# Kernel optimization log

Measured on AMD Instinct MI355X. Metric: run time of the kernel, lower is better.

Reference implementation:

```python
import jax, jax.numpy as jnp
import numpy as np

B, S, D, C = 2, 4096, 768, 8192
SCALE = 1.0
LN_EPS = 1e-5


def setup_inputs() -> dict:
    key = jax.random.key(0)
    ks = jax.random.split(key, 8)
    std = 0.03
    return {
        "x": jax.random.normal(ks[0], (B, S, D), dtype=jnp.float32),
        "attention_masks": jax.random.randint(ks[1], (B, S), 0, 2).astype(jnp.int32),
        "Wk": jax.random.normal(ks[2], (D, D), dtype=jnp.float32) * std,
        "Wv": jax.random.normal(ks[3], (D, D), dtype=jnp.float32) * std,
        "bv": jnp.zeros((D,), dtype=jnp.float32),
        "Q": jax.random.normal(ks[4], (C, D), dtype=jnp.float32) * std,  # label_representations
        "ln_gamma": jnp.ones((D,), dtype=jnp.float32),
        "ln_beta": jnp.zeros((D,), dtype=jnp.float32),
        "w_out": jax.random.normal(ks[5], (D,), dtype=jnp.float32) * std,  # output_linear.weight [1, D]
        "b_out": jnp.zeros((), dtype=jnp.float32),  # output_linear.bias [1]
    }


def reference(x, attention_masks, Wk, Wv, bv, Q, ln_gamma, ln_beta, w_out, b_out):
    # K, V projections (torch Linear: x @ W.T + b)
    K = jnp.einsum("bsd,ed->bse", x, Wk)
    V = jnp.einsum("bsd,ed->bse", x, Wv) + bv
    # label-query cross-attention scores: [B, C, S]
    scores = jnp.einsum("cd,bsd->bcs", Q, K)
    # additive mask: -inf where attention_masks == 0 (intended semantics of pad/repeat/masked_fill)
    scores = jnp.where(attention_masks[:, None, :] == 0, -jnp.inf, scores)
    attn = jax.nn.softmax(scores / SCALE, axis=2)  # [B, C, S]
    y = jnp.einsum("bcs,bsd->bcd", attn, V)  # [B, C, D]
    # LayerNorm over last dim
    mu = jnp.mean(y, axis=-1, keepdims=True)
    var = jnp.mean((y - mu) ** 2, axis=-1, keepdims=True)
    y = (y - mu) * jax.lax.rsqrt(var + LN_EPS) * ln_gamma + ln_beta
    # elementwise weight-mul-sum output head: [B, C]
    return jnp.einsum("bcd,d->bc", y, w_out) + b_out
```

## Files before the change

kernel.cpp:

```cpp
#include <hip/hip_runtime.h>
#include <hip/hip_bf16.h>
#include <hip/hip_fp16.h>

typedef _Float16 f16x8 __attribute__((ext_vector_type(8)));
typedef _Float16 f16x4 __attribute__((ext_vector_type(4)));
typedef float f32x4 __attribute__((ext_vector_type(4)));

#define AS1 __attribute__((address_space(1)))
#define AS3 __attribute__((address_space(3)))
#define MFMA16(a, b, c) __builtin_amdgcn_mfma_f32_16x16x32_f16(a, b, c, 0, 0, 0)

#define LDP 2304

__global__ __launch_bounds__(256) void maskscan(const int* __restrict__ am,
                                                int* __restrict__ idx,
                                                int* __restrict__ meta) {
  const int b = blockIdx.x, t = threadIdx.x;
  const int* m = am + (size_t)b * 4096;
  int* ix = idx + (size_t)b * 4096;
  __shared__ int cnt[256];
  __shared__ int pre[257];
  int loc[16], c = 0;
#pragma unroll
  for (int j = 0; j < 16; ++j) {
    loc[j] = m[t * 16 + j];
    c += (loc[j] != 0);
  }
  cnt[t] = c;
  __syncthreads();
  if (t == 0) {
    pre[0] = 0;
    for (int i = 0; i < 256; ++i) pre[i + 1] = pre[i] + cnt[i];
  }
  __syncthreads();
  int p = pre[t];
#pragma unroll
  for (int j = 0; j < 16; ++j)
    if (loc[j]) ix[p++] = t * 16 + j;
  const int valid = pre[256];
  int nsp = ((valid + 255) >> 8) << 8;
  if (nsp < 512) nsp = 512;
  for (int j = valid + t; j < nsp; j += 256) ix[j] = -1;
  if (t == 0) { meta[2 * b] = valid; meta[2 * b + 1] = nsp; }
}

__global__ __launch_bounds__(192) void gather_cvt(const float* __restrict__ x,
                                                  const int* __restrict__ idx,
                                                  const int* __restrict__ meta,
                                                  unsigned short* __restrict__ xc) {
  const int b = blockIdx.y, row = blockIdx.x, t = threadIdx.x;
  if (row >= meta[2 * b + 1]) return;
  const int src = idx[(size_t)b * 4096 + row];
  unsigned short* dst = xc + ((size_t)b * 4096 + row) * 768 + t * 4;
  f16x4 h;
  if (src < 0) {
    h[0] = h[1] = h[2] = h[3] = (_Float16)0.0f;
  } else {
    float4 v = *(const float4*)(x + ((size_t)b * 4096 + src) * 768 + t * 4);
    h[0] = (_Float16)v.x; h[1] = (_Float16)v.y; h[2] = (_Float16)v.z; h[3] = (_Float16)v.w;
  }
  *(f16x4*)dst = h;
}

__global__ __launch_bounds__(256) void cvt_f32_f16(const float* __restrict__ in,
                                                   unsigned short* __restrict__ out,
                                                   int n8) {
  int i = blockIdx.x * 256 + threadIdx.x;
  if (i >= n8) return;
  const float4* p = (const float4*)in + 2 * (size_t)i;
  float4 a = p[0], b = p[1];
  f16x8 h;
  h[0] = (_Float16)a.x; h[1] = (_Float16)a.y; h[2] = (_Float16)a.z; h[3] = (_Float16)a.w;
  h[4] = (_Float16)b.x; h[5] = (_Float16)b.y; h[6] = (_Float16)b.z; h[7] = (_Float16)b.w;
  *(f16x8*)(out + (size_t)i * 8) = h;
}

template <int OMODE, bool RBIAS, int EXITD>
__global__ __launch_bounds__(256) void gemm_nt(const unsigned short* __restrict__ A, int lda,
                                               const unsigned short* __restrict__ B, int ldb,
                                               void* __restrict__ Cout, int ldc,
                                               const float* __restrict__ bias,
                                               const int* __restrict__ meta,
                                               int N, int K) {
  const int nbn = N >> 7;
  const int bm = blockIdx.x / nbn, bn = blockIdx.x % nbn;
  if constexpr (EXITD == 1) {
    if (((bm & 31) << 7) >= meta[2 * (bm >> 5) + 1]) return;
  } else if constexpr (EXITD == 2) {
    if (((bn & 31) << 7) >= meta[2 * (bn >> 5) + 1]) return;
  }
  __shared__ __attribute__((aligned(16))) unsigned short As[128 * 64];
  __shared__ __attribute__((aligned(16))) unsigned short Bs[128 * 64];
  const int tid = threadIdx.x;
  const int w = tid >> 6, l = tid & 63;
  const int wr = w >> 1, wc = w & 1;
  const int lr = l & 15, lg = l >> 4;

  const unsigned short* Ab = A + (size_t)bm * 128 * lda;
  const unsigned short* Bb = B + (size_t)bn * 128 * ldb;

  f32x4 acc[4][4] = {};

  auto ldfrag = [&](const unsigned short* base, int row, int kk) {
    int off = row * 128 + kk * 64 + lg * 16;
    off ^= (row & 7) << 4;
    return *(const f16x8*)((const unsigned char*)base + off);
  };

  for (int kt = 0; kt < K; kt += 64) {
#pragma unroll
    for (int i = 0; i < 4; ++i) {
      const int c = i * 256 + w * 64 + l;
      const int row = c >> 3, col = (((c & 7) ^ (row & 7)) << 3);
      __builtin_amdgcn_global_load_lds((const AS1 void*)(Ab + (size_t)row * lda + kt + col),
                                       (AS3 void*)(As + (i * 256 + w * 64) * 8), 16, 0, 0);
    }
#pragma unroll
    for (int i = 0; i < 4; ++i) {
      const int c = i * 256 + w * 64 + l;
      const int row = c >> 3, col = (((c & 7) ^ (row & 7)) << 3);
      __builtin_amdgcn_global_load_lds((const AS1 void*)(Bb + (size_t)row * ldb + kt + col),
                                       (AS3 void*)(Bs + (i * 256 + w * 64) * 8), 16, 0, 0);
    }
    __syncthreads();
#pragma unroll
    for (int kk = 0; kk < 2; ++kk) {
      f16x8 af[4], bf[4];
#pragma unroll
      for (int mi = 0; mi < 4; ++mi) af[mi] = ldfrag(As, wr * 64 + mi * 16 + lr, kk);
#pragma unroll
      for (int ni = 0; ni < 4; ++ni) bf[ni] = ldfrag(Bs, wc * 64 + ni * 16 + lr, kk);
#pragma unroll
      for (int mi = 0; mi < 4; ++mi)
#pragma unroll
        for (int ni = 0; ni < 4; ++ni)
          acc[mi][ni] = MFMA16(af[mi], bf[ni], acc[mi][ni]);
    }
    __syncthreads();
  }

#pragma unroll
  for (int mi = 0; mi < 4; ++mi) {
#pragma unroll
    for (int r = 0; r < 4; ++r) {
      const int row = bm * 128 + wr * 64 + mi * 16 + lg * 4 + r;
      const float badd = RBIAS ? bias[row] : 0.0f;
#pragma unroll
      for (int ni = 0; ni < 4; ++ni) {
        const int col = bn * 128 + wc * 64 + ni * 16 + lr;
        float v = acc[mi][ni][r] + badd;
        if constexpr (OMODE == 0)
          ((unsigned short*)Cout)[(size_t)row * ldc + col] =
              __builtin_bit_cast(unsigned short, (_Float16)v);
        else
          ((float*)Cout)[(size_t)row * ldc + col] = v;
      }
    }
  }
}

#define VM8 asm volatile("s_waitcnt vmcnt(8)" ::: "memory")
#define VM4 asm volatile("s_waitcnt vmcnt(4)" ::: "memory")
#define VM0 asm volatile("s_waitcnt vmcnt(0)" ::: "memory")
#define VMNONE ((void)0)
#define BARRIER asm volatile("s_barrier" ::: "memory")

#define PH(kk, mh, VMW)                                                        \
  {                                                                            \
    f16x8 a0 = ldA8(4 * (mh) + 0, (kk));                                       \
    f16x8 a1 = ldA8(4 * (mh) + 1, (kk));                                       \
    f16x8 a2 = ldA8(4 * (mh) + 2, (kk));                                       \
    f16x8 a3 = ldA8(4 * (mh) + 3, (kk));                                       \
    f16x8 b0 = ldB8(0, (kk));                                                  \
    f16x8 b1 = ldB8(1, (kk));                                                  \
    f16x8 b2 = ldB8(2, (kk));                                                  \
    f16x8 b3 = ldB8(3, (kk));                                                  \
    if (u < NT4) stage(u);                                                     \
    ++u;                                                                       \
    BARRIER;                                                                   \
    __builtin_amdgcn_s_setprio(1);                                             \
    acc[4 * (mh) + 0][0] = MFMA16(a0, b0, acc[4 * (mh) + 0][0]);               \
    acc[4 * (mh) + 0][1] = MFMA16(a0, b1, acc[4 * (mh) + 0][1]);               \
    acc[4 * (mh) + 0][2] = MFMA16(a0, b2, acc[4 * (mh) + 0][2]);               \
    acc[4 * (mh) + 0][3] = MFMA16(a0, b3, acc[4 * (mh) + 0][3]);               \
    acc[4 * (mh) + 1][0] = MFMA16(a1, b0, acc[4 * (mh) + 1][0]);               \
    acc[4 * (mh) + 1][1] = MFMA16(a1, b1, acc[4 * (mh) + 1][1]);               \
    acc[4 * (mh) + 1][2] = MFMA16(a1, b2, acc[4 * (mh) + 1][2]);               \
    acc[4 * (mh) + 1][3] = MFMA16(a1, b3, acc[4 * (mh) + 1][3]);               \
    acc[4 * (mh) + 2][0] = MFMA16(a2, b0, acc[4 * (mh) + 2][0]);               \
    acc[4 * (mh) + 2][1] = MFMA16(a2, b1, acc[4 * (mh) + 2][1]);               \
    acc[4 * (mh) + 2][2] = MFMA16(a2, b2, acc[4 * (mh) + 2][2]);               \
    acc[4 * (mh) + 2][3] = MFMA16(a2, b3, acc[4 * (mh) + 2][3]);               \
    acc[4 * (mh) + 3][0] = MFMA16(a3, b0, acc[4 * (mh) + 3][0]);               \
    acc[4 * (mh) + 3][1] = MFMA16(a3, b1, acc[4 * (mh) + 3][1]);               \
    acc[4 * (mh) + 3][2] = MFMA16(a3, b2, acc[4 * (mh) + 3][2]);               \
    acc[4 * (mh) + 3][3] = MFMA16(a3, b3, acc[4 * (mh) + 3][3]);               \
    __builtin_amdgcn_s_setprio(0);                                             \
    VMW;                                                                       \
    BARRIER;                                                                   \
  }

template <int EPI>
__global__ __launch_bounds__(512, 2) void gemm256(
    const unsigned short* __restrict__ A, int lda, size_t sAz,
    const unsigned short* __restrict__ B, int ldb, size_t sBz,
    unsigned short* __restrict__ Cout, int ldc, size_t sCz, size_t sCk,
    const int* __restrict__ meta, int NTfix) {
  __shared__ __attribute__((aligned(16))) unsigned char lds[131072];
  const int tid = threadIdx.x;
  const int wv = tid >> 6, l = tid & 63;
  const int wm = wv >> 2, wn = wv & 3;
  const int lr = l & 15, lg = l >> 4;

  const int bid = blockIdx.x;
  int z, bm, bn, NT, koff, ks = 0;
  if constexpr (EPI == 2) {
    const int L0 = (meta[1] >> 8) << 5, L1 = (meta[3] >> 8) << 5;
    int idxq;
    if (bid < L0) { z = 0; idxq = bid; }
    else if (bid < L0 + L1) { z = 1; idxq = bid - L0; }
    else return;
    bm = idxq & 31;
    bn = idxq >> 5;
    NT = NTfix;
    koff = 0;
  } else {
    z = bid / 384;
    const int r = bid - z * 384;
    ks = r / 96;
    const int q = r - ks * 96;
    bm = q & 31;
    bn = q >> 5;
    const int nsp = meta[2 * z + 1];
    NT = nsp >> 8;
    koff = ks * (nsp >> 2);
  }
  const int valid = meta[2 * z];

  const unsigned short* Ab = A + (size_t)z * sAz + koff + (size_t)bm * 256 * lda;
  const unsigned short* Bb = B + (size_t)z * sBz + koff + (size_t)bn * 256 * ldb;

  const int NT4 = NT * 4;
  int bufOff = 0;

  auto stage = [&](int uu) {
    const int tau = uu >> 2, r = uu & 3;
    const int regionOff = ((tau & 1) << 16) | ((r & 1) << 15) | ((r >> 1) << 14);
    const unsigned short* base = (r & 1) ? Bb : Ab;
    const int ld = (r & 1) ? ldb : lda;
    const int kcol0 = tau * 64 + ((r >> 1) << 5);
#pragma unroll
    for (int j = 0; j < 2; ++j) {
      const int row = wv * 32 + j * 16 + (l >> 2);
      const int col = kcol0 + ((((l & 3) ^ ((row >> 1) & 3))) << 3);
      __builtin_amdgcn_global_load_lds(
          (const AS1 void*)(base + (size_t)row * ld + col),
          (AS3 void*)(lds + regionOff + wv * 2048 + j * 1024), 16, 0, 0);
    }
  };
  auto ldA8 = [&](int mf, int kk) {
    const int row = wm * 128 + mf * 16 + lr;
    int off = (row << 6) + (lg << 4);
    off ^= ((row >> 1) & 3) << 4;
    return *(const f16x8*)(lds + bufOff + (kk << 14) + off);
  };
  auto ldB8 = [&](int nf, int kk) {
    const int row = wn * 64 + nf * 16 + lr;
    int off = (row << 6) + (lg << 4);
    off ^= ((row >> 1) & 3) << 4;
    return *(const f16x8*)(lds + bufOff + 32768 + (kk << 14) + off);
  };

  f32x4 acc[8][4] = {};

  for (int i = 0; i < 6; ++i) stage(i);
  int u = 6;
  VM8;
  BARRIER;

  for (int t = 0; t + 2 < NT; ++t) {
    bufOff = (t & 1) << 16;
    PH(0, 0, VMNONE);
    PH(0, 1, VM8);
    PH(1, 0, VMNONE);
    PH(1, 1, VM8);
  }
  bufOff = ((NT - 2) & 1) << 16;
  PH(0, 0, VMNONE);
  PH(0, 1, VM8);
  PH(1, 0, VMNONE);
  PH(1, 1, VM4);
  bufOff = ((NT - 1) & 1) << 16;
  PH(0, 0, VMNONE);
  PH(0, 1, VM0);
  PH(1, 0, VMNONE);
  PH(1, 1, VMNONE);

  const size_t crow0 = (size_t)bm * 256 + wm * 128;
  const int ccol0 = bn * 256 + wn * 64;
  unsigned short* Cz = Cout + (size_t)z * sCz + (size_t)ks * sCk;
#pragma unroll
  for (int mf = 0; mf < 8; ++mf) {
#pragma unroll
    for (int rr = 0; rr < 4; ++rr) {
      const size_t rb = (crow0 + mf * 16 + lg * 4 + rr) * (size_t)ldc;
#pragma unroll
      for (int nf = 0; nf < 4; ++nf) {
        const int col = ccol0 + nf * 16 + lr;
        float v = acc[mf][nf][rr];
        if constexpr (EPI == 2) v = (col < valid) ? __expf(v) : 0.0f;
        Cz[rb + col] = __builtin_bit_cast(unsigned short, (_Float16)v);
      }
    }
  }
}

__device__ inline float block_sum(float v, float* sh, int t) {
#pragma unroll
  for (int o = 32; o; o >>= 1) v += __shfl_xor(v, o);
  __syncthreads();
  if ((t & 63) == 0) sh[t >> 6] = v;
  __syncthreads();
  return sh[0] + sh[1] + sh[2] + sh[3];
}

__global__ __launch_bounds__(256) void ln_head(const unsigned short* __restrict__ yp,
                                               size_t zoff, size_t koff,
                                               const float* __restrict__ gam,
                                               const float* __restrict__ bet,
                                               const float* __restrict__ wo,
                                               const float* __restrict__ bo,
                                               float* __restrict__ out) {
  const int z = blockIdx.y;
  const size_t rbase = (size_t)z * zoff + (size_t)blockIdx.x * 768;
  const _Float16* y0 = (const _Float16*)yp + rbase;
  const _Float16* y1 = y0 + koff;
  const _Float16* y2 = y1 + koff;
  const _Float16* y3 = y2 + koff;
  const int t = threadIdx.x;
  float a0 = (float)y0[t] + (float)y1[t] + (float)y2[t] + (float)y3[t];
  float a1 = (float)y0[t + 256] + (float)y1[t + 256] + (float)y2[t + 256] + (float)y3[t + 256];
  float a2 = (float)y0[t + 512] + (float)y1[t + 512] + (float)y2[t + 512] + (float)y3[t + 512];
  __shared__ float sh[4];
  float s = block_sum(a0 + a1 + a2, sh, t);
  float mu = s * (1.0f / 768.0f);
  float d0 = a0 - mu, d1 = a1 - mu, d2 = a2 - mu;
  float q = block_sum(d0 * d0 + d1 * d1 + d2 * d2, sh, t);
  float rs = rsqrtf(q * (1.0f / 768.0f) + 1e-5f);
  float o = (d0 * rs * gam[t] + bet[t]) * wo[t] +
            (d1 * rs * gam[t + 256] + bet[t + 256]) * wo[t + 256] +
            (d2 * rs * gam[t + 512] + bet[t + 512]) * wo[t + 512];
  o = block_sum(o, sh, t);
  if (t == 0) out[(size_t)z * 8192 + blockIdx.x] = o + bo[0];
}

extern "C" void kernel_launch(void* const* d_in, const int* in_sizes, int n_in,
                              void* d_out, int out_size, void* d_ws, size_t ws_size,
                              hipStream_t stream) {
  const float* x  = (const float*)d_in[0];
  const int*   am = (const int*)d_in[1];
  const float* Wk = (const float*)d_in[2];
  const float* Wv = (const float*)d_in[3];
  const float* bv = (const float*)d_in[4];
  const float* Q  = (const float*)d_in[5];
  const float* gam = (const float*)d_in[6];
  const float* bet = (const float*)d_in[7];
  const float* wo  = (const float*)d_in[8];
  const float* bo  = (const float*)d_in[9];
  float* out = (float*)d_out;

  const int S = 4096, D = 768, C = 8192;
  const size_t nX = (size_t)2 * S * D;
  const size_t nW = (size_t)D * D;
  const size_t nQ = (size_t)C * D;
  const size_t nPc = (size_t)C * LDP;
  const size_t nY = (size_t)C * D;

  unsigned short* xc  = (unsigned short*)d_ws;
  unsigned short* Wkb = xc + nX;
  unsigned short* Wvb = Wkb + nW;
  unsigned short* Qb  = Wvb + nW;
  unsigned short* Kb  = Qb + nQ;
  unsigned short* Vt  = Kb + nX;
  unsigned short* P   = Vt + nX;
  unsigned short* yp  = P + 2 * nPc;
  int* idx  = (int*)(yp + 8 * nY);
  int* meta = idx + 2 * 4096;

  maskscan<<<2, 256, 0, stream>>>(am, idx, meta);
  gather_cvt<<<dim3(4096, 2), 192, 0, stream>>>(x, idx, meta, xc);

  cvt_f32_f16<<<(int)(nW / 8 / 256), 256, 0, stream>>>(Wk, Wkb, (int)(nW / 8));
  cvt_f32_f16<<<(int)(nW / 8 / 256), 256, 0, stream>>>(Wv, Wvb, (int)(nW / 8));
  cvt_f32_f16<<<(int)(nQ / 8 / 256), 256, 0, stream>>>(Q, Qb, (int)(nQ / 8));

  gemm_nt<0, false, 1><<<(8192 / 128) * (768 / 128), 256, 0, stream>>>(
      xc, D, Wkb, D, Kb, D, nullptr, meta, 768, D);
  gemm_nt<0, true, 2><<<(768 / 128) * (8192 / 128), 256, 0, stream>>>(
      Wvb, D, xc, D, Vt, 2 * S, bv, meta, 2 * S, D);

  gemm256<2><<<dim3(1024, 1), 512, 0, stream>>>(
      Qb, D, 0, Kb, D, (size_t)S * D, P, LDP, nPc, 0, meta, 12);

  gemm256<0><<<dim3(768, 1), 512, 0, stream>>>(
      P, LDP, nPc, Vt, 2 * S, (size_t)S, yp, D, 4 * nY, nY, meta, 0);

  ln_head<<<dim3(C, 2), 256, 0, stream>>>(yp, 4 * nY, nY, gam, bet, wo, bo, out);
}
```

Baseline: 243.1 us.

## Make score GEMM persistent over two tile passes and halve split-K for PV GEMM

The QK^T score GEMM now launches 512 blocks, each handling up to two output tiles in sequence: a first pass over the first 8 column tiles per batch, then the remaining valid tiles. Before, a launch of 1024 blocks had many early exits. The P·V GEMM drops split-K from 4 to 2, so it uses 384 blocks, writes half as many partial buffers, and LN reads two partials instead of four. The goal is less launch, tail and partial-sum traffic, at the cost of fewer concurrent blocks and longer per-block K loops.

Measured after the change: 234.3 us. -3.6%, faster.

```diff
diff --git a/kernel.cpp b/kernel.cpp
--- a/kernel.cpp
+++ b/kernel.cpp
@@ -213,34 +213,9 @@
   const int lr = l & 15, lg = l >> 4;
 
   const int bid = blockIdx.x;
-  int z, bm, bn, NT, koff, ks = 0;
-  if constexpr (EPI == 2) {
-    const int L0 = (meta[1] >> 8) << 5, L1 = (meta[3] >> 8) << 5;
-    int idxq;
-    if (bid < L0) { z = 0; idxq = bid; }
-    else if (bid < L0 + L1) { z = 1; idxq = bid - L0; }
-    else return;
-    bm = idxq & 31;
-    bn = idxq >> 5;
-    NT = NTfix;
-    koff = 0;
-  } else {
-    z = bid / 384;
-    const int r = bid - z * 384;
-    ks = r / 96;
-    const int q = r - ks * 96;
-    bm = q & 31;
-    bn = q >> 5;
-    const int nsp = meta[2 * z + 1];
-    NT = nsp >> 8;
-    koff = ks * (nsp >> 2);
-  }
-  const int valid = meta[2 * z];
-
-  const unsigned short* Ab = A + (size_t)z * sAz + koff + (size_t)bm * 256 * lda;
-  const unsigned short* Bb = B + (size_t)z * sBz + koff + (size_t)bn * 256 * ldb;
-
-  const int NT4 = NT * 4;
+
+  const unsigned short* Ab = nullptr;
+  const unsigned short* Bb = nullptr;
   int bufOff = 0;
 
   auto stage = [&](int uu) {
@@ -271,45 +246,86 @@
     return *(const f16x8*)(lds + bufOff + 32768 + (kk << 14) + off);
   };
 
-  f32x4 acc[8][4] = {};
-
-  for (int i = 0; i < 6; ++i) stage(i);
-  int u = 6;
-  VM8;
-  BARRIER;
-
-  for (int t = 0; t + 2 < NT; ++t) {
-    bufOff = (t & 1) << 16;
+  constexpr int NPASS = (EPI == 2) ? 2 : 1;
+
+  for (int pass = 0; pass < NPASS; ++pass) {
+    int z, bm, bn, NT, koff, ks = 0;
+    if constexpr (EPI == 2) {
+      if (pass == 0) {
+        z = bid >> 8;
+        const int rem = bid & 255;
+        bm = rem & 31;
+        bn = rem >> 5;
+        if (bn * 256 >= meta[2 * z + 1]) continue;
+      } else {
+        const int tn0 = max(0, (meta[1] >> 8) - 8);
+        const int tn1 = max(0, (meta[3] >> 8) - 8);
+        if (bid >= 32 * (tn0 + tn1)) break;
+        int t = bid;
+        if (t < 32 * tn0) { z = 0; }
+        else { t -= 32 * tn0; z = 1; }
+        bm = t & 31;
+        bn = 8 + (t >> 5);
+      }
+      NT = NTfix;
+      koff = 0;
+    } else {
+      z = bid / 192;
+      const int r = bid - z * 192;
+      ks = r / 96;
+      const int q = r - ks * 96;
+      bm = q & 31;
+      bn = q >> 5;
+      const int nsp = meta[2 * z + 1];
+      NT = nsp >> 7;
+      koff = ks * (nsp >> 1);
+    }
+    const int valid = meta[2 * z];
+
+    Ab = A + (size_t)z * sAz + koff + (size_t)bm * 256 * lda;
+    Bb = B + (size_t)z * sBz + koff + (size_t)bn * 256 * ldb;
+
+    const int NT4 = NT * 4;
+    f32x4 acc[8][4] = {};
+
+    for (int i = 0; i < 6; ++i) stage(i);
+    int u = 6;
+    VM8;
+    BARRIER;
+
+    for (int t = 0; t + 2 < NT; ++t) {
+      bufOff = (t & 1) << 16;
+      PH(0, 0, VMNONE);
+      PH(0, 1, VM8);
+      PH(1, 0, VMNONE);
+      PH(1, 1, VM8);
+    }
+    bufOff = ((NT - 2) & 1) << 16;
     PH(0, 0, VMNONE);
     PH(0, 1, VM8);
     PH(1, 0, VMNONE);
-    PH(1, 1, VM8);
-  }
-  bufOff = ((NT - 2) & 1) << 16;
-  PH(0, 0, VMNONE);
-  PH(0, 1, VM8);
-  PH(1, 0, VMNONE);
-  PH(1, 1, VM4);
-  bufOff = ((NT - 1) & 1) << 16;
-  PH(0, 0, VMNONE);
-  PH(0, 1, VM0);
-  PH(1, 0, VMNONE);
-  PH(1, 1, VMNONE);
-
-  const size_t crow0 = (size_t)bm * 256 + wm * 128;
-  const int ccol0 = bn * 256 + wn * 64;
-  unsigned short* Cz = Cout + (size_t)z * sCz + (size_t)ks * sCk;
-#pragma unroll
-  for (int mf = 0; mf < 8; ++mf) {
-#pragma unroll
-    for (int rr = 0; rr < 4; ++rr) {
-      const size_t rb = (crow0 + mf * 16 + lg * 4 + rr) * (size_t)ldc;
-#pragma unroll
-      for (int nf = 0; nf < 4; ++nf) {
-        const int col = ccol0 + nf * 16 + lr;
-        float v = acc[mf][nf][rr];
-        if constexpr (EPI == 2) v = (col < valid) ? __expf(v) : 0.0f;
-        Cz[rb + col] = __builtin_bit_cast(unsigned short, (_Float16)v);
+    PH(1, 1, VM4);
+    bufOff = ((NT - 1) & 1) << 16;
+    PH(0, 0, VMNONE);
+    PH(0, 1, VM0);
+    PH(1, 0, VMNONE);
+    PH(1, 1, VMNONE);
+
+    const size_t crow0 = (size_t)bm * 256 + wm * 128;
+    const int ccol0 = bn * 256 + wn * 64;
+    unsigned short* Cz = Cout + (size_t)z * sCz + (size_t)ks * sCk;
+#pragma unroll
+    for (int mf = 0; mf < 8; ++mf) {
+#pragma unroll
+      for (int rr = 0; rr < 4; ++rr) {
+        const size_t rb = (crow0 + mf * 16 + lg * 4 + rr) * (size_t)ldc;
+#pragma unroll
+        for (int nf = 0; nf < 4; ++nf) {
+          const int col = ccol0 + nf * 16 + lr;
+          float v = acc[mf][nf][rr];
+          if constexpr (EPI == 2) v = (col < valid) ? __expf(v) : 0.0f;
+          Cz[rb + col] = __builtin_bit_cast(unsigned short, (_Float16)v);
+        }
       }
     }
   }
@@ -335,12 +351,10 @@
   const size_t rbase = (size_t)z * zoff + (size_t)blockIdx.x * 768;
   const _Float16* y0 = (const _Float16*)yp + rbase;
   const _Float16* y1 = y0 + koff;
-  const _Float16* y2 = y1 + koff;
-  const _Float16* y3 = y2 + koff;
   const int t = threadIdx.x;
-  float a0 = (float)y0[t] + (float)y1[t] + (float)y2[t] + (float)y3[t];
-  float a1 = (float)y0[t + 256] + (float)y1[t + 256] + (float)y2[t + 256] + (float)y3[t + 256];
-  float a2 = (float)y0[t + 512] + (float)y1[t + 512] + (float)y2[t + 512] + (float)y3[t + 512];
+  float a0 = (float)y0[t] + (float)y1[t];
+  float a1 = (float)y0[t + 256] + (float)y1[t + 256];
+  float a2 = (float)y0[t + 512] + (float)y1[t + 512];
   __shared__ float sh[4];
   float s = block_sum(a0 + a1 + a2, sh, t);
   float mu = s * (1.0f / 768.0f);
@@ -384,7 +398,7 @@
   unsigned short* Vt  = Kb + nX;
   unsigned short* P   = Vt + nX;
   unsigned short* yp  = P + 2 * nPc;
-  int* idx  = (int*)(yp + 8 * nY);
+  int* idx  = (int*)(yp + 4 * nY);
   int* meta = idx + 2 * 4096;
 
   maskscan<<<2, 256, 0, stream>>>(am, idx, meta);
@@ -399,11 +413,11 @@
   gemm_nt<0, true, 2><<<(768 / 128) * (8192 / 128), 256, 0, stream>>>(
       Wvb, D, xc, D, Vt, 2 * S, bv, meta, 2 * S, D);
 
-  gemm256<2><<<dim3(1024, 1), 512, 0, stream>>>(
+  gemm256<2><<<dim3(512, 1), 512, 0, stream>>>(
       Qb, D, 0, Kb, D, (size_t)S * D, P, LDP, nPc, 0, meta, 12);
 
-  gemm256<0><<<dim3(768, 1), 512, 0, stream>>>(
-      P, LDP, nPc, Vt, 2 * S, (size_t)S, yp, D, 4 * nY, nY, meta, 0);
-
-  ln_head<<<dim3(C, 2), 256, 0, stream>>>(yp, 4 * nY, nY, gam, bet, wo, bo, out);
-}
+  gemm256<0><<<dim3(384, 1), 512, 0, stream>>>(
+      P, LDP, nPc, Vt, 2 * S, (size_t)S, yp, D, 2 * nY, nY, meta, 0);
+
+  ln_head<<<dim3(C, 2), 256, 0, stream>>>(yp, 2 * nY, nY, gam, bet, wo, bo, out);
+}
```
